# Kernel optimization log

Hardware: AMD Instinct MI355X
Metric: run time of the kernel (lower is better)

## Reference

```python
import jax, jax.numpy as jnp
import numpy as np

HID = 512
NUM_NODES = 100000
N_BATCH = 20000


def _gru_cell(x, h, W_ih, W_hh, b_ih, b_hh):
    # torch nn.GRU single-step cell; gate order r, z, n
    gi = x @ W_ih.T + b_ih            # [N, 3H]
    gh = h @ W_hh.T + b_hh            # [N, 3H]
    i_r, i_z, i_n = jnp.split(gi, 3, axis=-1)
    h_r, h_z, h_n = jnp.split(gh, 3, axis=-1)
    r = jax.nn.sigmoid(i_r + h_r)
    z = jax.nn.sigmoid(i_z + h_z)
    n = jnp.tanh(i_n + r * h_n)
    return (1.0 - z) * n + z * h


def setup_inputs() -> dict:
    key = jax.random.key(0)
    ks = jax.random.split(key, 12)
    s = 1.0 / np.sqrt(HID)
    inp = {
        'conv_emb': jax.random.normal(ks[0], (N_BATCH, HID), jnp.float32),
        'static_table': jax.random.normal(ks[1], (NUM_NODES, HID), jnp.float32),
        'dynamic_table': jax.random.normal(ks[2], (NUM_NODES, 2, HID), jnp.float32),
        'W_ih0': jax.random.normal(ks[3], (3 * HID, 2 * HID), jnp.float32) * s,
        'W_hh0': jax.random.normal(ks[4], (3 * HID, HID), jnp.float32) * s,
        'b_ih0': jax.random.normal(ks[5], (3 * HID,), jnp.float32) * s,
        'b_hh0': jax.random.normal(ks[6], (3 * HID,), jnp.float32) * s,
        'W_ih1': jax.random.normal(ks[7], (3 * HID, HID), jnp.float32) * s,
        'W_hh1': jax.random.normal(ks[8], (3 * HID, HID), jnp.float32) * s,
        'b_ih1': jax.random.normal(ks[9], (3 * HID,), jnp.float32) * s,
        'b_hh1': jax.random.normal(ks[10], (3 * HID,), jnp.float32) * s,
        'nids': jnp.arange(N_BATCH, dtype=jnp.int32),  # unique global node ids
    }
    return inp


def reference(conv_emb, static_table, dynamic_table,
              W_ih0, W_hh0, b_ih0, b_hh0,
              W_ih1, W_hh1, b_ih1, b_hh1, nids):
    # gather: static embeddings for batch nodes, concat with conv output
    x = jnp.concatenate([conv_emb, static_table[nids]], axis=-1)  # [N, 2H]
    h0 = dynamic_table[nids]                                      # [N, L, H]
    # single-step 2-layer GRU (seq_len == 1)
    h_new0 = _gru_cell(x, h0[:, 0], W_ih0, W_hh0, b_ih0, b_hh0)   # [N, H]
    h_new1 = _gru_cell(h_new0, h0[:, 1], W_ih1, W_hh1, b_ih1, b_hh1)
    hn = jnp.stack([h_new0, h_new1], axis=1)                      # [N, L, H]
    # scatter updated hidden states back into the persistent table
    updated_table = dynamic_table.at[nids].set(hn)                # [num_nodes, L, H]
    return updated_table
```

## Files before the change

kernel.cpp:

```cpp
#include <hip/hip_runtime.h>

#define NB 20000
#define NNODES 100000
#define MB2 79
#define MP2 (MB2*256)

typedef unsigned short u16;
typedef __bf16 bf16x8 __attribute__((ext_vector_type(8)));
typedef float f32x4 __attribute__((ext_vector_type(4)));

__device__ __forceinline__ u16 f2bf(float f) {
  union { float f; unsigned u; } v; v.f = f;
  unsigned r = v.u + 0x7fffu + ((v.u >> 16) & 1u);
  return (u16)(r >> 16);
}
__device__ __forceinline__ float bf2f(u16 b) {
  union { unsigned u; float f; } v; v.u = ((unsigned)b) << 16;
  return v.f;
}

template <int N> __device__ __forceinline__ void vmwaitc() {
  if constexpr (N == 0) asm volatile("s_waitcnt vmcnt(0)" ::: "memory");
  else if constexpr (N == 2) asm volatile("s_waitcnt vmcnt(2)" ::: "memory");
  else if constexpr (N == 4) asm volatile("s_waitcnt vmcnt(4)" ::: "memory");
  else asm volatile("s_waitcnt vmcnt(8)" ::: "memory");
  __builtin_amdgcn_sched_barrier(0);
}
__device__ __forceinline__ void bar() {
  __builtin_amdgcn_sched_barrier(0);
  __builtin_amdgcn_s_barrier();
  __builtin_amdgcn_sched_barrier(0);
}

__global__ void prep_bt0i(const float* __restrict__ Wih, const float* __restrict__ Whh,
                          u16* __restrict__ Bt) {
  int idx = blockIdx.x * 256 + threadIdx.x;
  if (idx >= 2048 * 384) return;
  int jg = idx / 384;
  int k = (idx % 384) * 4;
  int j = jg >> 2, g = jg & 3;
  float4 v = make_float4(0.f, 0.f, 0.f, 0.f);
  if (g < 2) {
    int row = g * 512 + j;
    v = (k < 1024) ? *(const float4*)(Wih + (size_t)row * 1024 + k)
                   : *(const float4*)(Whh + (size_t)row * 512 + (k - 1024));
  } else if (g == 2) {
    if (k < 1024) v = *(const float4*)(Wih + (size_t)(1024 + j) * 1024 + k);
  } else {
    if (k >= 1024) v = *(const float4*)(Whh + (size_t)(1024 + j) * 512 + (k - 1024));
  }
  ushort4 b; b.x = f2bf(v.x); b.y = f2bf(v.y); b.z = f2bf(v.z); b.w = f2bf(v.w);
  *(ushort4*)(Bt + (size_t)jg * 1536 + k) = b;
}

__global__ void prep_bt1i(const float* __restrict__ Wih, const float* __restrict__ Whh,
                          u16* __restrict__ Bt) {
  int idx = blockIdx.x * 256 + threadIdx.x;
  if (idx >= 2048 * 256) return;
  int jg = idx / 256;
  int k = (idx % 256) * 4;
  int j = jg >> 2, g = jg & 3;
  float4 v = make_float4(0.f, 0.f, 0.f, 0.f);
  if (g < 2) {
    int row = g * 512 + j;
    v = (k < 512) ? *(const float4*)(Wih + (size_t)row * 512 + k)
                  : *(const float4*)(Whh + (size_t)row * 512 + (k - 512));
  } else if (g == 2) {
    if (k < 512) v = *(const float4*)(Wih + (size_t)(1024 + j) * 512 + k);
  } else {
    if (k >= 512) v = *(const float4*)(Whh + (size_t)(1024 + j) * 512 + (k - 512));
  }
  ushort4 b; b.x = f2bf(v.x); b.y = f2bf(v.y); b.z = f2bf(v.z); b.w = f2bf(v.w);
  *(ushort4*)(Bt + (size_t)jg * 1024 + k) = b;
}

__global__ void prep_a(const float* __restrict__ conv, const float* __restrict__ stat,
                       const float* __restrict__ dyn, const int* __restrict__ nids,
                       u16* __restrict__ A0, u16* __restrict__ A1) {
  int idx = blockIdx.x * 256 + threadIdx.x;
  int n = idx >> 9;
  int c = (idx & 511) * 4;
  if (n >= MP2) return;
  float4 v = make_float4(0.f, 0.f, 0.f, 0.f);
  if (n < NB) {
    size_t nid = (size_t)nids[n];
    if (c < 512)        v = *(const float4*)(conv + (size_t)n * 512 + c);
    else if (c < 1024)  v = *(const float4*)(stat + nid * 512 + (c - 512));
    else if (c < 1536)  v = *(const float4*)(dyn + nid * 1024 + (c - 1024));
    else                v = *(const float4*)(dyn + nid * 1024 + 512 + (c - 1536));
  }
  ushort4 b; b.x = f2bf(v.x); b.y = f2bf(v.y); b.z = f2bf(v.z); b.w = f2bf(v.w);
  if (c < 1536) *(ushort4*)(A0 + (size_t)n * 1536 + c) = b;
  else          *(ushort4*)(A1 + (size_t)n * 1024 + (c - 1024)) = b;
  if (n >= NB && c < 512) *(ushort4*)(A1 + (size_t)n * 1024 + c) = b;
}

template <int K, bool DUAL>
__global__ __launch_bounds__(512, 2)
void gemm8(const u16* __restrict__ A, const u16* __restrict__ Bt,
           const float* __restrict__ bih, const float* __restrict__ bhh,
           const u16* __restrict__ hsrc, int hstride,
           u16* __restrict__ o1, u16* __restrict__ o2) {
  constexpr int NT = K / 64;
  __shared__ u16 S[4][16384];

  int bid = blockIdx.x;
  int gidx = (bid & 7) * MB2 + (bid >> 3);
  int bm = gidx >> 3, bn = gidx & 7;

  int t = threadIdx.x;
  int lane = t & 63, w = t >> 6;
  int fr = lane & 15, fq = lane >> 4;
  int wm4 = w & 3, wn = w >> 2;

  const u16* Ap = A + (size_t)bm * 256 * K;
  const u16* Bp = Bt + (size_t)bn * 256 * K;

  f32x4 acc[2][2][2][4] = {};

  auto stage = [&](int kt2, int mat, int half, const u16* gsrc) {
#pragma unroll
    for (int l = 0; l < 2; ++l) {
      int row = half * 128 + l * 64 + (t >> 3);
      int gx = ((t & 7) * 16) ^ ((row & 7) << 4);
      const u16* g = gsrc + (size_t)row * K + kt2 * 64 + (gx >> 1);
      char* lp = (char*)&S[(kt2 & 1) * 2 + mat][0] + half * 16384 + l * 8192 + t * 16;
      __builtin_amdgcn_global_load_lds((const __attribute__((address_space(1))) void*)g,
                                       (__attribute__((address_space(3))) void*)lp, 16, 0, 0);
    }
  };
  auto ld = [&](int buf, int mat, int row, int kb) -> bf16x8 {
    return *(const bf16x8*)((const char*)&S[buf * 2 + mat][0] + row * 128 +
                            (kb ^ ((row & 7) << 4)));
  };

  stage(0, 0, 0, Ap); stage(0, 1, 0, Bp); stage(0, 1, 1, Bp); stage(0, 0, 1, Ap);
  stage(1, 0, 0, Ap); stage(1, 1, 0, Bp);
  vmwaitc<8>();
  bar();

  for (int kt = 0; kt < NT; ++kt) {
    int cur = kt & 1;
#pragma unroll
    for (int q = 0; q < 4; ++q) {
      const int mh = q >> 1, nh = q & 1;
      bf16x8 af[2][2], bv[4][2];
#pragma unroll
      for (int mi = 0; mi < 2; ++mi)
#pragma unroll
        for (int ks = 0; ks < 2; ++ks)
          af[mi][ks] = ld(cur, 0, mh * 128 + wm4 * 32 + mi * 16 + fr, ks * 64 + fq * 16);
#pragma unroll
      for (int nf = 0; nf < 4; ++nf)
#pragma unroll
        for (int ks = 0; ks < 2; ++ks)
          bv[nf][ks] = ld(cur, 1, nh * 128 + wn * 64 + nf * 16 + fr, ks * 64 + fq * 16);

      if (q == 0)      { if (kt + 1 < NT) stage(kt + 1, 1, 1, Bp); }
      else if (q == 1) { if (kt + 1 < NT) stage(kt + 1, 0, 1, Ap); }
      else if (q == 2) { if (kt + 2 < NT) stage(kt + 2, 0, 0, Ap); }
      else             { if (kt + 2 < NT) stage(kt + 2, 1, 0, Bp); }

      bar();
      __builtin_amdgcn_s_setprio(1);
#pragma unroll
      for (int mi = 0; mi < 2; ++mi)
#pragma unroll
        for (int nf = 0; nf < 4; ++nf)
#pragma unroll
          for (int ks = 0; ks < 2; ++ks)
            acc[mh][nh][mi][nf] = __builtin_amdgcn_mfma_f32_16x16x32_bf16(
                af[mi][ks], bv[nf][ks], acc[mh][nh][mi][nf], 0, 0, 0);
      __builtin_amdgcn_s_setprio(0);

      if (q == 0)      { if (kt + 1 < NT) vmwaitc<8>(); else vmwaitc<2>(); }
      else if (q == 1) { if (kt + 1 < NT) vmwaitc<8>(); else vmwaitc<0>(); }
      else if (q == 3) { if (kt + 1 < NT) { if (kt + 2 < NT) vmwaitc<8>(); else vmwaitc<4>(); } }
      bar();
    }
  }

  int gg = fr & 3, jj = fr >> 2;
  float bias[2][4];
#pragma unroll
  for (int nh = 0; nh < 2; ++nh)
#pragma unroll
    for (int nf = 0; nf < 4; ++nf) {
      int j = ((bn * 256 + nh * 128 + wn * 64 + nf * 16) >> 2) + jj;
      bias[nh][nf] = (gg == 0) ? bih[j] + bhh[j]
                   : (gg == 1) ? bih[512 + j] + bhh[512 + j]
                   : (gg == 2) ? bih[1024 + j] : bhh[1024 + j];
    }
#pragma unroll
  for (int mh = 0; mh < 2; ++mh)
#pragma unroll
    for (int nh = 0; nh < 2; ++nh)
#pragma unroll
      for (int mi = 0; mi < 2; ++mi) {
        int row = bm * 256 + mh * 128 + wm4 * 32 + mi * 16 + fq * 4 + gg;
#pragma unroll
        for (int nf = 0; nf < 4; ++nf) {
          float v[4], v1[4], v2[4];
#pragma unroll
          for (int r = 0; r < 4; ++r) v[r] = acc[mh][nh][mi][nf][r] + bias[nh][nf];
#pragma unroll
          for (int i = 0; i < 4; ++i) {
            float o = __shfl_xor(v[i ^ 2], 2);
            v1[i] = ((i ^ gg) & 2) ? o : v[i];
          }
#pragma unroll
          for (int i = 0; i < 4; ++i) {
            float o = __shfl_xor(v1[i ^ 1], 1);
            v2[i] = ((i ^ gg) & 1) ? o : v1[i];
          }
          if (row < NB) {
            int j = ((bn * 256 + nh * 128 + wn * 64 + nf * 16) >> 2) + jj;
            float rr = 1.f / (1.f + __expf(-v2[0]));
            float zz = 1.f / (1.f + __expf(-v2[1]));
            float nn = tanhf(fmaf(rr, v2[3], v2[2]));
            float h = bf2f(hsrc[(size_t)row * hstride + j]);
            float hp = (1.f - zz) * nn + zz * h;
            u16 hb = f2bf(hp);
            if (DUAL) { o1[(size_t)row * 1024 + j] = hb; o2[(size_t)row * 512 + j] = hb; }
            else      { o1[(size_t)row * 512 + j] = hb; }
          }
        }
      }
}

__global__ void init_inv(int* __restrict__ inv) {
  int i = blockIdx.x * 256 + threadIdx.x;
  if (i < NNODES) inv[i] = -1;
}
__global__ void set_inv(const int* __restrict__ nids, int* __restrict__ inv) {
  int i = blockIdx.x * 256 + threadIdx.x;
  if (i < NB) inv[nids[i]] = i;
}
__global__ void assemble(const float4* __restrict__ dyn4, const u16* __restrict__ H0,
                         const u16* __restrict__ H1, const int* __restrict__ inv,
                         float4* __restrict__ out4) {
  const size_t total = (size_t)NNODES * 256;
  for (size_t i = (size_t)blockIdx.x * 256 + threadIdx.x; i < total;
       i += (size_t)gridDim.x * 256) {
    int row = (int)(i >> 8);
    int n = inv[row];
    if (n < 0) {
      out4[i] = dyn4[i];
    } else {
      int c = (int)(i & 255) * 4;
      const u16* s = (c < 512) ? H0 + (size_t)n * 512 + c : H1 + (size_t)n * 512 + (c - 512);
      float4 v; v.x = bf2f(s[0]); v.y = bf2f(s[1]); v.z = bf2f(s[2]); v.w = bf2f(s[3]);
      out4[i] = v;
    }
  }
}

extern "C" void kernel_launch(void* const* d_in, const int* in_sizes, int n_in,
                              void* d_out, int out_size, void* d_ws, size_t ws_size,
                              hipStream_t stream) {
  const float* conv = (const float*)d_in[0];
  const float* stat = (const float*)d_in[1];
  const float* dyn  = (const float*)d_in[2];
  const float* Wih0 = (const float*)d_in[3];
  const float* Whh0 = (const float*)d_in[4];
  const float* bih0 = (const float*)d_in[5];
  const float* bhh0 = (const float*)d_in[6];
  const float* Wih1 = (const float*)d_in[7];
  const float* Whh1 = (const float*)d_in[8];
  const float* bih1 = (const float*)d_in[9];
  const float* bhh1 = (const float*)d_in[10];
  const int*   nids = (const int*)d_in[11];

  char* ws = (char*)d_ws;
  u16* A0  = (u16*)ws;
  u16* H0b = (u16*)(ws + 62128128);
  u16* Bt0 = (u16*)(ws + 82837504);
  u16* Bt1 = (u16*)(ws + 89128960);
  u16* H1  = (u16*)ws;
  int* inv = (int*)(ws + 82837504);
  u16* A1  = (u16*)d_out;

  prep_bt0i<<<3072, 256, 0, stream>>>(Wih0, Whh0, Bt0);
  prep_bt1i<<<2048, 256, 0, stream>>>(Wih1, Whh1, Bt1);
  prep_a<<<(MP2 * 512) / 256, 256, 0, stream>>>(conv, stat, dyn, nids, A0, A1);

  gemm8<1536, true><<<MB2 * 8, 512, 0, stream>>>(A0, Bt0, bih0, bhh0,
                                                 A0 + 1024, 1536, A1, H0b);

  init_inv<<<(NNODES + 255) / 256, 256, 0, stream>>>(inv);
  set_inv<<<(NB + 255) / 256, 256, 0, stream>>>(nids, inv);

  gemm8<1024, false><<<MB2 * 8, 512, 0, stream>>>(A1, Bt1, bih1, bhh1,
                                                  A1 + 512, 1024, H1, (u16*)nullptr);

  assemble<<<4096, 256, 0, stream>>>((const float4*)dyn, H0b, H1, inv, (float4*)d_out);
}
```

Baseline: 527.3 us.

## Fuse output scatter into GEMM epilogues and overlap table copy with GEMMs

The separate assemble pass and inverse-index map are replaced by a bitmask of updated rows. Each GEMM epilogue now writes fp32 hidden states directly to output rows via nids. The bulk copy of untouched table rows is split into extra blocks appended to each GEMM grid plus a small tail kernel, so the memory-bound copy can overlap with the compute-bound GEMMs. A1 moves from the output buffer into workspace, which enlarges workspace use, and the copy split boundaries are hardcoded row ratios.

```diff
diff --git a/kernel.cpp b/kernel.cpp
--- a/kernel.cpp
+++ b/kernel.cpp
@@ -4,6 +4,9 @@
 #define NNODES 100000
 #define MB2 79
 #define MP2 (MB2*256)
+#define NBITW 3125
+#define NGEMM (MB2*8)
+#define NCOPY 1416
 
 typedef unsigned short u16;
 typedef __bf16 bf16x8 __attribute__((ext_vector_type(8)));
@@ -95,14 +98,51 @@
   if (n >= NB && c < 512) *(ushort4*)(A1 + (size_t)n * 1024 + c) = b;
 }
 
-template <int K, bool DUAL>
+__global__ void zero_bits(unsigned* __restrict__ bits) {
+  int i = blockIdx.x * 256 + threadIdx.x;
+  if (i < NBITW) bits[i] = 0;
+}
+__global__ void set_bits(const int* __restrict__ nids, unsigned* __restrict__ bits) {
+  int i = blockIdx.x * 256 + threadIdx.x;
+  if (i < NB) {
+    int nid = nids[i];
+    atomicOr(&bits[nid >> 5], 1u << (nid & 31));
+  }
+}
+
+template <int K, int LAYER>
 __global__ __launch_bounds__(512, 2)
 void gemm8(const u16* __restrict__ A, const u16* __restrict__ Bt,
            const float* __restrict__ bih, const float* __restrict__ bhh,
-           const u16* __restrict__ hsrc, int hstride,
-           u16* __restrict__ o1, u16* __restrict__ o2) {
+           const u16* __restrict__ hsrc, int hstride, const int* __restrict__ nids,
+           u16* __restrict__ a1out, float* __restrict__ out,
+           const float4* __restrict__ src4, float4* __restrict__ dst4,
+           const unsigned* __restrict__ bits, long cbeg, long cend) {
   constexpr int NT = K / 64;
   __shared__ u16 S[4][16384];
+
+  if (blockIdx.x >= NGEMM) {
+    long cb = blockIdx.x - NGEMM;
+    long total = cend - cbeg;
+    long per = (total + NCOPY - 1) / NCOPY;
+    long s = cbeg + cb * per;
+    long e = s + per; if (e > cend) e = cend;
+    long i = s + threadIdx.x;
+    for (; i + 1536 < e; i += 2048) {
+      float4 a0 = src4[i], a1 = src4[i + 512], a2 = src4[i + 1024], a3 = src4[i + 1536];
+      int r0 = (int)(i >> 8), r1 = (int)((i + 512) >> 8),
+          r2 = (int)((i + 1024) >> 8), r3 = (int)((i + 1536) >> 8);
+      if (!((bits[r0 >> 5] >> (r0 & 31)) & 1u)) dst4[i] = a0;
+      if (!((bits[r1 >> 5] >> (r1 & 31)) & 1u)) dst4[i + 512] = a1;
+      if (!((bits[r2 >> 5] >> (r2 & 31)) & 1u)) dst4[i + 1024] = a2;
+      if (!((bits[r3 >> 5] >> (r3 & 31)) & 1u)) dst4[i + 1536] = a3;
+    }
+    for (; i < e; i += 512) {
+      int row = (int)(i >> 8);
+      if (!((bits[row >> 5] >> (row & 31)) & 1u)) dst4[i] = src4[i];
+    }
+    return;
+  }
 
   int bid = blockIdx.x;
   int gidx = (bid & 7) * MB2 + (bid >> 3);
@@ -220,38 +260,19 @@
             float nn = tanhf(fmaf(rr, v2[3], v2[2]));
             float h = bf2f(hsrc[(size_t)row * hstride + j]);
             float hp = (1.f - zz) * nn + zz * h;
-            u16 hb = f2bf(hp);
-            if (DUAL) { o1[(size_t)row * 1024 + j] = hb; o2[(size_t)row * 512 + j] = hb; }
-            else      { o1[(size_t)row * 512 + j] = hb; }
+            if (LAYER == 0) a1out[(size_t)row * 1024 + j] = f2bf(hp);
+            out[(size_t)nids[row] * 1024 + LAYER * 512 + j] = hp;
           }
         }
       }
 }
 
-__global__ void init_inv(int* __restrict__ inv) {
-  int i = blockIdx.x * 256 + threadIdx.x;
-  if (i < NNODES) inv[i] = -1;
-}
-__global__ void set_inv(const int* __restrict__ nids, int* __restrict__ inv) {
-  int i = blockIdx.x * 256 + threadIdx.x;
-  if (i < NB) inv[nids[i]] = i;
-}
-__global__ void assemble(const float4* __restrict__ dyn4, const u16* __restrict__ H0,
-                         const u16* __restrict__ H1, const int* __restrict__ inv,
-                         float4* __restrict__ out4) {
-  const size_t total = (size_t)NNODES * 256;
-  for (size_t i = (size_t)blockIdx.x * 256 + threadIdx.x; i < total;
-       i += (size_t)gridDim.x * 256) {
+__global__ void copy_tail(const float4* __restrict__ src, float4* __restrict__ dst,
+                          const unsigned* __restrict__ bits, long cbeg, long cend) {
+  for (long i = cbeg + (long)blockIdx.x * 256 + threadIdx.x; i < cend;
+       i += (long)gridDim.x * 256) {
     int row = (int)(i >> 8);
-    int n = inv[row];
-    if (n < 0) {
-      out4[i] = dyn4[i];
-    } else {
-      int c = (int)(i & 255) * 4;
-      const u16* s = (c < 512) ? H0 + (size_t)n * 512 + c : H1 + (size_t)n * 512 + (c - 512);
-      float4 v; v.x = bf2f(s[0]); v.y = bf2f(s[1]); v.z = bf2f(s[2]); v.w = bf2f(s[3]);
-      out4[i] = v;
-    }
+    if (!((bits[row >> 5] >> (row & 31)) & 1u)) dst[i] = src[i];
   }
 }
 
@@ -270,28 +291,28 @@
   const float* bih1 = (const float*)d_in[9];
   const float* bhh1 = (const float*)d_in[10];
   const int*   nids = (const int*)d_in[11];
+  float* out = (float*)d_out;
 
   char* ws = (char*)d_ws;
   u16* A0  = (u16*)ws;
-  u16* H0b = (u16*)(ws + 62128128);
-  u16* Bt0 = (u16*)(ws + 82837504);
-  u16* Bt1 = (u16*)(ws + 89128960);
-  u16* H1  = (u16*)ws;
-  int* inv = (int*)(ws + 82837504);
-  u16* A1  = (u16*)d_out;
-
+  u16* A1  = (u16*)(ws + 62128128);
+  u16* Bt0 = (u16*)(ws + 103546880);
+  u16* Bt1 = (u16*)(ws + 109838336);
+  unsigned* bits = (unsigned*)(ws + 114032640);
+
+  zero_bits<<<(NBITW + 255) / 256, 256, 0, stream>>>(bits);
+  set_bits<<<(NB + 255) / 256, 256, 0, stream>>>(nids, bits);
   prep_bt0i<<<3072, 256, 0, stream>>>(Wih0, Whh0, Bt0);
   prep_bt1i<<<2048, 256, 0, stream>>>(Wih1, Whh1, Bt1);
   prep_a<<<(MP2 * 512) / 256, 256, 0, stream>>>(conv, stat, dyn, nids, A0, A1);
 
-  gemm8<1536, true><<<MB2 * 8, 512, 0, stream>>>(A0, Bt0, bih0, bhh0,
-                                                 A0 + 1024, 1536, A1, H0b);
-
-  init_inv<<<(NNODES + 255) / 256, 256, 0, stream>>>(inv);
-  set_inv<<<(NB + 255) / 256, 256, 0, stream>>>(nids, inv);
-
-  gemm8<1024, false><<<MB2 * 8, 512, 0, stream>>>(A1, Bt1, bih1, bhh1,
-                                                  A1 + 512, 1024, H1, (u16*)nullptr);
-
-  assemble<<<4096, 256, 0, stream>>>((const float4*)dyn, H0b, H1, inv, (float4*)d_out);
-}
+  const long E_ROW = 256;
+  gemm8<1536, 0><<<NGEMM + NCOPY, 512, 0, stream>>>(
+      A0, Bt0, bih0, bhh0, A0 + 1024, 1536, nids, A1, out,
+      (const float4*)dyn, (float4*)out, bits, 0L, 55000L * E_ROW);
+  gemm8<1024, 1><<<NGEMM + NCOPY, 512, 0, stream>>>(
+      A1, Bt1, bih1, bhh1, A1 + 512, 1024, nids, (u16*)nullptr, out,
+      (const float4*)dyn, (float4*)out, bits, 55000L * E_ROW, 92000L * E_ROW);
+  copy_tail<<<1024, 256, 0, stream>>>((const float4*)dyn, (float4*)out, bits,
+                                      92000L * E_ROW, (long)NNODES * E_ROW);
+}
```

Result: faster. 510.2 us (-3.2%).
